# Kernel tuning notes

Hardware: AMD Instinct MI355X
Metric: run time of the kernel (lower is better)

## Reference

```python
import jax, jax.numpy as jnp
import numpy as np

N = 50000          # nodes
E = 1_600_000      # edges (avg degree 32)
IN = 128           # in_channels
H1, C1 = 4, 8      # conv1: heads=4, out=8 -> concat 32
OUT = 64           # out_channels (conv2, heads=1)
NEG_SLOPE = 0.2    # PyG GATConv default LeakyReLU slope


def _gat_layer(x, edge_index, W, att_src, att_dst, bias, heads, out_ch):
    """PyG-style GATConv (concat=True, add_self_loops=True).
    x: [N, F_in], edge_index: [2, E], W: [F_in, heads*out_ch],
    att_src/att_dst: [heads, out_ch], bias: [heads*out_ch].
    """
    n = x.shape[0]
    loops = jnp.arange(n)
    src = jnp.concatenate([edge_index[0], loops])  # message source j
    dst = jnp.concatenate([edge_index[1], loops])  # aggregation target i

    h = (x @ W).reshape(n, heads, out_ch)                 # [N, H, C]
    a_src = jnp.sum(h * att_src, axis=-1)                 # [N, H]
    a_dst = jnp.sum(h * att_dst, axis=-1)                 # [N, H]

    logits = jax.nn.leaky_relu(a_src[src] + a_dst[dst], NEG_SLOPE)  # [E', H]
    # segment softmax over incoming edges of each destination node
    m = jax.ops.segment_max(logits, dst, num_segments=n)            # [N, H]
    e = jnp.exp(logits - m[dst])
    s = jax.ops.segment_sum(e, dst, num_segments=n)                 # [N, H]
    alpha = e / (s[dst] + 1e-16)                                    # [E', H]

    msg = h[src] * alpha[..., None]                                 # [E', H, C]
    out = jax.ops.segment_sum(msg, dst, num_segments=n)             # [N, H, C]
    return out.reshape(n, heads * out_ch) + bias


def setup_inputs() -> dict:
    key = jax.random.key(0)
    ks = jax.random.split(key, 10)
    g = 0.1
    x = jax.random.normal(ks[0], (N, IN), jnp.float32)
    edge_index = jax.random.randint(ks[1], (2, E), 0, N, dtype=jnp.int64)
    W1 = jax.random.normal(ks[2], (IN, H1 * C1), jnp.float32) * g
    att_src1 = jax.random.normal(ks[3], (H1, C1), jnp.float32) * g
    att_dst1 = jax.random.normal(ks[4], (H1, C1), jnp.float32) * g
    b1 = jnp.zeros((H1 * C1,), jnp.float32)
    W2 = jax.random.normal(ks[5], (H1 * C1, OUT), jnp.float32) * g
    att_src2 = jax.random.normal(ks[6], (1, OUT), jnp.float32) * g
    att_dst2 = jax.random.normal(ks[7], (1, OUT), jnp.float32) * g
    b2 = jnp.zeros((OUT,), jnp.float32)
    return {"x": x, "edge_index": edge_index,
            "W1": W1, "att_src1": att_src1, "att_dst1": att_dst1, "b1": b1,
            "W2": W2, "att_src2": att_src2, "att_dst2": att_dst2, "b2": b2}


def reference(x, edge_index, W1, att_src1, att_dst1, b1, W2, att_src2, att_dst2, b2):
    h = _gat_layer(x, edge_index, W1, att_src1, att_dst1, b1, H1, C1)   # [N, 32]
    h = jax.nn.relu(h)
    out = _gat_layer(h, edge_index, W2, att_src2, att_dst2, b2, 1, OUT)  # [N, 64]
    return out
```

## Files before the change

### kernel.cpp

```cpp
#include <hip/hip_runtime.h>
#include <hip/hip_bf16.h>

#define IN_CH 128
#define H1C1  32
#define NH1   4
#define OUTC  64
#define NEG   0.2f
#define RPAD  16
#define BSH   6
#define BSZ   64
#define NBMAX 1024
#define CHUNK 4096
#define CAP   3072
#define PCAP  4096
#define NPB   32

typedef __hip_bfloat16 bf16;
typedef unsigned int u32;
typedef unsigned short u16;

__device__ __forceinline__ u16 f2bf_bits(float f) {
  bf16 v = __float2bfloat16(f);
  return *(u16*)&v;
}
__device__ __forceinline__ float bflo(u32 g) { return __uint_as_float(g << 16); }
__device__ __forceinline__ float bfhi(u32 g) { return __uint_as_float(g & 0xFFFF0000u); }

__global__ __launch_bounds__(256) void k_bin_tr(
    const int* __restrict__ ei, int* __restrict__ bucket_fill,
    u32* __restrict__ data, int E, int n, int nb, int nA,
    const float* __restrict__ x, const float* __restrict__ W1,
    const float* __restrict__ as1, const float* __restrict__ ad1,
    u16* __restrict__ h1b, float* __restrict__ a_src, float* __restrict__ a_dst) {
  __shared__ __align__(16) char smem[28672];
  int t = threadIdx.x;
  if ((int)blockIdx.x < nA) {
    int* cnt   = (int*)smem;
    int* lbase = cnt + NBMAX;
    int* gbase = lbase + NBMAX;
    u32* staged = (u32*)(gbase + NBMAX);
    int lane = t & 63, wid = t >> 6;
    for (int b = t; b < nb; b += 256) cnt[b] = 0;
    __syncthreads();
    long base = (long)blockIdx.x * CHUNK;
    long totE = (long)E + n;
    u32 pk[CHUNK / 256];
    int bk[CHUNK / 256];
#pragma unroll
    for (int i = 0; i < CHUNK / 256; i++) {
      long e = base + i * 256 + t;
      if (e < totE) {
        int j, d;
        if (e < E) {
          j = ei[e]; d = ei[E + e];
          j = j < 0 ? 0 : (j >= n ? n - 1 : j);
          d = d < 0 ? 0 : (d >= n ? n - 1 : d);
        } else { j = d = (int)(e - E); }
        bk[i] = d >> BSH;
        pk[i] = ((u32)d << 16) | (u32)j;
        atomicAdd(&cnt[bk[i]], 1);
      } else bk[i] = -1;
    }
    __syncthreads();
    if (wid == 0) {
      int carry = 0;
      for (int b0 = 0; b0 < nb; b0 += 64) {
        int i = b0 + lane;
        int v = (i < nb) ? cnt[i] : 0;
        int orig = v;
        for (int off = 1; off < 64; off <<= 1) {
          int u = __shfl_up(v, off, 64);
          if (lane >= off) v += u;
        }
        if (i < nb) lbase[i] = carry + v - orig;
        carry += __shfl(v, 63, 64);
      }
    }
    __syncthreads();
    for (int b = t; b < nb; b += 256) {
      int c = cnt[b];
      gbase[b] = c ? atomicAdd(&bucket_fill[b], c) : 0;
      cnt[b] = 0;
    }
    __syncthreads();
#pragma unroll
    for (int i = 0; i < CHUNK / 256; i++) {
      if (bk[i] >= 0) {
        int loc = atomicAdd(&cnt[bk[i]], 1);
        staged[lbase[bk[i]] + loc] = pk[i];
      }
    }
    __syncthreads();
    long remL = totE - base;
    int rem = remL > CHUNK ? CHUNK : (int)remL;
    for (int idx = t; idx < rem; idx += 256) {
      u32 p = staged[idx];
      int b = (int)(p >> 16) >> BSH;
      int off2 = gbase[b] + (idx - lbase[b]);
      if (off2 < CAP) data[(size_t)b * CAP + off2] = p;
    }
  } else {
    float* xs = (float*)smem;
    int base = ((int)blockIdx.x - nA) * NPB;
    for (int i4 = t; i4 < NPB * 32; i4 += 256) {
      int nd = base + (i4 >> 5);
      float4 v = make_float4(0.f, 0.f, 0.f, 0.f);
      if (nd < n) v = ((const float4*)x)[(size_t)base * 32 + i4];
      ((float4*)xs)[i4] = v;
    }
    int mg = t & 7, ks = (t >> 3) & 7, ns = t >> 6;
    int m0 = mg * 4;
    float4 w[4][4];
#pragma unroll
    for (int kk = 0; kk < 4; kk++) {
      int q = (kk + ks) & 3;
      int k0 = ks * 16 + q * 4;
      float4 t0 = *(const float4*)(W1 + (k0 + 0) * H1C1 + m0);
      float4 t1 = *(const float4*)(W1 + (k0 + 1) * H1C1 + m0);
      float4 t2 = *(const float4*)(W1 + (k0 + 2) * H1C1 + m0);
      float4 t3 = *(const float4*)(W1 + (k0 + 3) * H1C1 + m0);
      w[kk][0] = make_float4(t0.x, t1.x, t2.x, t3.x);
      w[kk][1] = make_float4(t0.y, t1.y, t2.y, t3.y);
      w[kk][2] = make_float4(t0.z, t1.z, t2.z, t3.z);
      w[kk][3] = make_float4(t0.w, t1.w, t2.w, t3.w);
    }
    float4 asq = *(const float4*)(as1 + m0);
    float4 adq = *(const float4*)(ad1 + m0);
    __syncthreads();
#pragma unroll 2
    for (int r = 0; r < 8; r++) {
      int nl = r * 4 + ns;
      const float4* xrow = (const float4*)(xs + nl * IN_CH + ks * 16);
      float a0 = 0.f, a1 = 0.f, a2 = 0.f, a3 = 0.f;
#pragma unroll
      for (int kk = 0; kk < 4; kk++) {
        int q = (kk + ks) & 3;
        float4 xv = xrow[q];
        a0 += xv.x * w[kk][0].x + xv.y * w[kk][0].y + xv.z * w[kk][0].z + xv.w * w[kk][0].w;
        a1 += xv.x * w[kk][1].x + xv.y * w[kk][1].y + xv.z * w[kk][1].z + xv.w * w[kk][1].w;
        a2 += xv.x * w[kk][2].x + xv.y * w[kk][2].y + xv.z * w[kk][2].z + xv.w * w[kk][2].w;
        a3 += xv.x * w[kk][3].x + xv.y * w[kk][3].y + xv.z * w[kk][3].z + xv.w * w[kk][3].w;
      }
#pragma unroll
      for (int off = 8; off < 64; off <<= 1) {
        a0 += __shfl_xor(a0, off, 64);
        a1 += __shfl_xor(a1, off, 64);
        a2 += __shfl_xor(a2, off, 64);
        a3 += __shfl_xor(a3, off, 64);
      }
      int node = base + nl;
      if (ks == 0 && node < n) {
        float vs = a0 * asq.x + a1 * asq.y + a2 * asq.z + a3 * asq.w;
        float vd = a0 * adq.x + a1 * adq.y + a2 * adq.z + a3 * adq.w;
        vs += __shfl_xor(vs, 1, 64);
        vd += __shfl_xor(vd, 1, 64);
        u32 lo = (u32)f2bf_bits(a0) | ((u32)f2bf_bits(a1) << 16);
        u32 hi = (u32)f2bf_bits(a2) | ((u32)f2bf_bits(a3) << 16);
        *(uint2*)(h1b + (size_t)node * H1C1 + m0) = make_uint2(lo, hi);
        if ((mg & 1) == 0) {
          a_src[node * NH1 + (mg >> 1)] = vs;
          a_dst[node * NH1 + (mg >> 1)] = vd;
        }
      }
    }
    if ((int)blockIdx.x == nA) {
      if (t < H1C1) h1b[n * H1C1 + t] = 0;
      if (t < NH1)  a_src[n * NH1 + t] = -1e30f;
    }
  }
}

__global__ __launch_bounds__(256) void k_bucket_scatter(
    const u32* __restrict__ data, const int* __restrict__ bucket_fill,
    int2* __restrict__ rowse, int* __restrict__ col, int n) {
  __shared__ int cur[BSZ];
  __shared__ int rp[BSZ];
  __shared__ int pd[BSZ];
  int t = threadIdx.x;
  int b = blockIdx.x;
  if (t < BSZ) cur[t] = 0;
  __syncthreads();
  int s = b * CAP;
  int cnt = bucket_fill[b];
  if (cnt > CAP) cnt = CAP;
  for (int i = t; i < cnt; i += 256)
    atomicAdd(&cur[(data[s + i] >> 16) & (BSZ - 1)], 1);
  __syncthreads();
  if (t < 64) {
    int raw = cur[t];
    int v = (raw + RPAD - 1) & ~(RPAD - 1);
    int orig = v;
    for (int off = 1; off < 64; off <<= 1) {
      int u = __shfl_up(v, off, 64);
      if (t >= off) v += u;
    }
    int r = b * PCAP + v - orig;
    rp[t] = r;
    pd[t] = orig;
    cur[t] = r;
    int node = (b << BSH) + t;
    if (node < n) rowse[node] = make_int2(r, r + orig);
  }
  __syncthreads();
  for (int i = t; i < cnt; i += 256) {
    u32 p = data[s + i];
    int dl = (int)(p >> 16) & (BSZ - 1);
    int pos = atomicAdd(&cur[dl], 1);
    col[pos] = (int)(p & 0xFFFFu);
  }
  __syncthreads();
  if (t < 64) {
    int c = cur[t];
    int end = rp[t] + pd[t];
    for (int k = c; k < end; k++) col[k] = n;
  }
}

__global__ __launch_bounds__(256) void k_l1_agg(
    const int2* __restrict__ rowse, const int* __restrict__ col,
    const u16* __restrict__ h1b, const float* __restrict__ a_src,
    const float* __restrict__ a_dst, const float* __restrict__ b1,
    const float* __restrict__ W2, const float* __restrict__ as2,
    const float* __restrict__ ad2,
    u16* __restrict__ h2, float* __restrict__ a_src2, float* __restrict__ a_dst2,
    int n) {
  __shared__ float W2s[8 * 256];
  __shared__ float hsh[16][H1C1];
  __shared__ int   js[4][4][64];
  __shared__ float wsh[4][4][NH1][68];
  int t = threadIdx.x;
  int wid = t >> 6, lane = t & 63;
  {
    int c = t & 63;
#pragma unroll
    for (int g = 0; g < 2; g++) {
      int kg = (t >> 6) + 4 * g;
      float4 v;
      v.x = W2[(kg * 4 + 0) * OUTC + c];
      v.y = W2[(kg * 4 + 1) * OUTC + c];
      v.z = W2[(kg * 4 + 2) * OUTC + c];
      v.w = W2[(kg * 4 + 3) * OUTC + c];
      *(float4*)(W2s + kg * 256 + c * 4) = v;
    }
  }
  int o = lane >> 3, u = lane & 7;
  int hd = u >> 1;
  const char* h1p = (const char*)h1b + 8 * u;
  int node0 = blockIdx.x * 16 + wid * 4;
  int rs[4], re[4], jv[4];
  float4 adv[4];
#pragma unroll
  for (int s = 0; s < 4; s++) {
    int nd = node0 + s;
    int2 se = make_int2(0, 0);
    if (nd < n) se = rowse[nd];
    rs[s] = se.x; re[s] = se.y;
  }
#pragma unroll
  for (int s = 0; s < 4; s++) {
    int k1 = re[s] - rs[s]; if (k1 > 64) k1 = 64;
    jv[s] = (lane < k1) ? col[rs[s] + lane] : n;
  }
#pragma unroll
  for (int s = 0; s < 4; s++) {
    int nd = node0 + s; int ndc = nd < n ? nd : 0;
    adv[s] = *(const float4*)(a_dst + ndc * NH1);
  }
  float4 asv[4];
#pragma unroll
  for (int s = 0; s < 4; s++) asv[s] = *(const float4*)(a_src + jv[s] * NH1);
#pragma unroll
  for (int s = 0; s < 4; s++) {
    float l0 = asv[s].x + adv[s].x; l0 = l0 > 0.f ? l0 : NEG * l0;
    float l1 = asv[s].y + adv[s].y; l1 = l1 > 0.f ? l1 : NEG * l1;
    float l2 = asv[s].z + adv[s].z; l2 = l2 > 0.f ? l2 : NEG * l2;
    float l3 = asv[s].w + adv[s].w; l3 = l3 > 0.f ? l3 : NEG * l3;
    js[wid][s][lane] = jv[s] << 6;
    wsh[wid][s][0][lane] = __expf(l0);
    wsh[wid][s][1][lane] = __expf(l1);
    wsh[wid][s][2][lane] = __expf(l2);
    wsh[wid][s][3][lane] = __expf(l3);
  }
#pragma unroll
  for (int s = 0; s < 4; s++) {
    float a0 = 0.f, a1 = 0.f, a2 = 0.f, a3 = 0.f, sw = 0.f;
    int k1 = re[s] - rs[s]; if (k1 > 64) k1 = 64;
    int nbod = k1 >> 4;
    uint2 G0[4], G1[4];
    float W0[4], W1v[4];
#pragma unroll
    for (int b = 0; b < 4; b++) {
      if (b < nbod) {
        int k = b * 16;
        int j0 = js[wid][s][k + o];
        int j1 = js[wid][s][k + 8 + o];
        W0[b]  = wsh[wid][s][hd][k + o];
        W1v[b] = wsh[wid][s][hd][k + 8 + o];
        G0[b] = *(const uint2*)(h1p + j0);
        G1[b] = *(const uint2*)(h1p + j1);
      }
    }
#pragma unroll
    for (int b = 0; b < 4; b++) {
      if (b < nbod) {
        float w0 = W0[b], w1 = W1v[b];
        uint2 g0 = G0[b], g1 = G1[b];
        a0 += w0 * bflo(g0.x) + w1 * bflo(g1.x);
        a1 += w0 * bfhi(g0.x) + w1 * bfhi(g1.x);
        a2 += w0 * bflo(g0.y) + w1 * bflo(g1.y);
        a3 += w0 * bfhi(g0.y) + w1 * bfhi(g1.y);
        sw += w0 + w1;
      }
    }
    for (int tb = rs[s] + 64; tb < re[s]; tb += 64) {
      int kmax = re[s] - tb; if (kmax > 64) kmax = 64;
      int jx = (lane < kmax) ? col[tb + lane] : n;
      float4 as = *(const float4*)(a_src + jx * NH1);
      float l0 = as.x + adv[s].x; l0 = l0 > 0.f ? l0 : NEG * l0;
      float l1 = as.y + adv[s].y; l1 = l1 > 0.f ? l1 : NEG * l1;
      float l2 = as.z + adv[s].z; l2 = l2 > 0.f ? l2 : NEG * l2;
      float l3 = as.w + adv[s].w; l3 = l3 > 0.f ? l3 : NEG * l3;
      js[wid][s][lane] = jx << 6;
      wsh[wid][s][0][lane] = __expf(l0);
      wsh[wid][s][1][lane] = __expf(l1);
      wsh[wid][s][2][lane] = __expf(l2);
      wsh[wid][s][3][lane] = __expf(l3);
      int nb2 = kmax >> 4;
#pragma unroll
      for (int b = 0; b < 4; b++) {
        if (b < nb2) {
          int k = b * 16;
          int j0 = js[wid][s][k + o];
          int j1 = js[wid][s][k + 8 + o];
          float w0 = wsh[wid][s][hd][k + o];
          float w1 = wsh[wid][s][hd][k + 8 + o];
          uint2 g0 = *(const uint2*)(h1p + j0);
          uint2 g1 = *(const uint2*)(h1p + j1);
          a0 += w0 * bflo(g0.x) + w1 * bflo(g1.x);
          a1 += w0 * bfhi(g0.x) + w1 * bfhi(g1.x);
          a2 += w0 * bflo(g0.y) + w1 * bflo(g1.y);
          a3 += w0 * bfhi(g0.y) + w1 * bfhi(g1.y);
          sw += w0 + w1;
        }
      }
    }
    for (int off = 8; off < 64; off <<= 1) {
      a0 += __shfl_xor(a0, off, 64);
      a1 += __shfl_xor(a1, off, 64);
      a2 += __shfl_xor(a2, off, 64);
      a3 += __shfl_xor(a3, off, 64);
      sw += __shfl_xor(sw, off, 64);
    }
    if (o == 0) {
      float inv = 1.f / (sw + 1e-16f);
      int c = 4 * u;
      hsh[wid * 4 + s][c]     = fmaxf(a0 * inv + b1[c], 0.f);
      hsh[wid * 4 + s][c + 1] = fmaxf(a1 * inv + b1[c + 1], 0.f);
      hsh[wid * 4 + s][c + 2] = fmaxf(a2 * inv + b1[c + 2], 0.f);
      hsh[wid * 4 + s][c + 3] = fmaxf(a3 * inv + b1[c + 3], 0.f);
    }
  }
  __syncthreads();
  float as2l = as2[lane], ad2l = ad2[lane];
  for (int r = 0; r < 4; r++) {
    int nl = wid * 4 + r;
    int node = blockIdx.x * 16 + nl;
    float acc = 0.f;
#pragma unroll
    for (int kg = 0; kg < 8; kg++) {
      float4 hv = *(const float4*)(&hsh[nl][kg * 4]);
      float4 wv = *(const float4*)(W2s + kg * 256 + lane * 4);
      acc += hv.x * wv.x + hv.y * wv.y + hv.z * wv.z + hv.w * wv.w;
    }
    float vs = acc * as2l;
    float vd = acc * ad2l;
    for (int off = 1; off < 64; off <<= 1) {
      vs += __shfl_xor(vs, off, 64);
      vd += __shfl_xor(vd, off, 64);
    }
    if (node < n) {
      h2[node * OUTC + lane] = f2bf_bits(acc);
      if (lane == 0) { a_src2[node] = vs; a_dst2[node] = vd; }
    }
  }
  if (blockIdx.x == 0) {
    if (t < OUTC) h2[n * OUTC + t] = 0;
    if (t == 0)   a_src2[n] = -1e30f;
  }
}

__global__ __launch_bounds__(256) void k_l2_agg(
    const int2* __restrict__ rowse, const int* __restrict__ col,
    const u16* __restrict__ h2, const float* __restrict__ a_src2,
    const float* __restrict__ a_dst2, const float* __restrict__ b2v,
    float* __restrict__ out, int n) {
  __shared__ int   js[4][4][64];
  __shared__ float wsh[4][4][64];
  int t = threadIdx.x;
  int wid = t >> 6, lane = t & 63;
  int o = lane >> 4, u = lane & 15;
  const char* h2p = (const char*)h2 + 8 * u;
  int node0 = blockIdx.x * 16 + wid * 4;
  int rs[4], re[4], jv[4];
  float adv[4];
#pragma unroll
  for (int s = 0; s < 4; s++) {
    int nd = node0 + s;
    int2 se = make_int2(0, 0);
    if (nd < n) se = rowse[nd];
    rs[s] = se.x; re[s] = se.y;
  }
#pragma unroll
  for (int s = 0; s < 4; s++) {
    int k1 = re[s] - rs[s]; if (k1 > 64) k1 = 64;
    jv[s] = (lane < k1) ? col[rs[s] + lane] : n;
  }
#pragma unroll
  for (int s = 0; s < 4; s++) {
    int nd = node0 + s; int ndc = nd < n ? nd : 0;
    adv[s] = a_dst2[ndc];
  }
  float asv[4];
#pragma unroll
  for (int s = 0; s < 4; s++) asv[s] = a_src2[jv[s]];
#pragma unroll
  for (int s = 0; s < 4; s++) {
    float lg = asv[s] + adv[s];
    lg = lg > 0.f ? lg : NEG * lg;
    js[wid][s][lane] = jv[s] << 7;
    wsh[wid][s][lane] = __expf(lg);
  }
#pragma unroll
  for (int s = 0; s < 4; s++) {
    int node = node0 + s;
    float a0 = 0.f, a1 = 0.f, a2 = 0.f, a3 = 0.f, sw = 0.f;
    int k1 = re[s] - rs[s]; if (k1 > 64) k1 = 64;
    int nbod = k1 >> 4;
    uint2 G[4][4];
    float W[4][4];
#pragma unroll
    for (int b = 0; b < 4; b++) {
      if (b < nbod) {
#pragma unroll
        for (int q = 0; q < 4; q++) {
          int e = b * 16 + 4 * q + o;
          W[b][q] = wsh[wid][s][e];
          G[b][q] = *(const uint2*)(h2p + js[wid][s][e]);
        }
      }
    }
#pragma unroll
    for (int b = 0; b < 4; b++) {
      if (b < nbod) {
        a0 += W[b][0] * bflo(G[b][0].x) + W[b][1] * bflo(G[b][1].x);
        a0 += W[b][2] * bflo(G[b][2].x) + W[b][3] * bflo(G[b][3].x);
        a1 += W[b][0] * bfhi(G[b][0].x) + W[b][1] * bfhi(G[b][1].x);
        a1 += W[b][2] * bfhi(G[b][2].x) + W[b][3] * bfhi(G[b][3].x);
        a2 += W[b][0] * bflo(G[b][0].y) + W[b][1] * bflo(G[b][1].y);
        a2 += W[b][2] * bflo(G[b][2].y) + W[b][3] * bflo(G[b][3].y);
        a3 += W[b][0] * bfhi(G[b][0].y) + W[b][1] * bfhi(G[b][1].y);
        a3 += W[b][2] * bfhi(G[b][2].y) + W[b][3] * bfhi(G[b][3].y);
        sw += (W[b][0] + W[b][1]) + (W[b][2] + W[b][3]);
      }
    }
    for (int tb = rs[s] + 64; tb < re[s]; tb += 64) {
      int kmax = re[s] - tb; if (kmax > 64) kmax = 64;
      int jx = (lane < kmax) ? col[tb + lane] : n;
      float lg = a_src2[jx] + adv[s];
      lg = lg > 0.f ? lg : NEG * lg;
      js[wid][s][lane] = jx << 7;
      wsh[wid][s][lane] = __expf(lg);
      int nb2 = kmax >> 4;
#pragma unroll
      for (int b = 0; b < 4; b++) {
        if (b < nb2) {
          float w0, w1, w2, w3;
          uint2 g0, g1, g2, g3;
          int k = b * 16;
          w0 = wsh[wid][s][k + o];      g0 = *(const uint2*)(h2p + js[wid][s][k + o]);
          w1 = wsh[wid][s][k + 4 + o];  g1 = *(const uint2*)(h2p + js[wid][s][k + 4 + o]);
          w2 = wsh[wid][s][k + 8 + o];  g2 = *(const uint2*)(h2p + js[wid][s][k + 8 + o]);
          w3 = wsh[wid][s][k + 12 + o]; g3 = *(const uint2*)(h2p + js[wid][s][k + 12 + o]);
          a0 += w0 * bflo(g0.x) + w1 * bflo(g1.x) + w2 * bflo(g2.x) + w3 * bflo(g3.x);
          a1 += w0 * bfhi(g0.x) + w1 * bfhi(g1.x) + w2 * bfhi(g2.x) + w3 * bfhi(g3.x);
          a2 += w0 * bflo(g0.y) + w1 * bflo(g1.y) + w2 * bflo(g2.y) + w3 * bflo(g3.y);
          a3 += w0 * bfhi(g0.y) + w1 * bfhi(g1.y) + w2 * bfhi(g2.y) + w3 * bfhi(g3.y);
          sw += (w0 + w1) + (w2 + w3);
        }
      }
    }
    for (int off = 16; off < 64; off <<= 1) {
      a0 += __shfl_xor(a0, off, 64);
      a1 += __shfl_xor(a1, off, 64);
      a2 += __shfl_xor(a2, off, 64);
      a3 += __shfl_xor(a3, off, 64);
      sw += __shfl_xor(sw, off, 64);
    }
    if (o == 0 && node < n) {
      float inv = 1.f / (sw + 1e-16f);
      int c = 4 * u;
      float4 ov;
      ov.x = a0 * inv + b2v[c];
      ov.y = a1 * inv + b2v[c + 1];
      ov.z = a2 * inv + b2v[c + 2];
      ov.w = a3 * inv + b2v[c + 3];
      *(float4*)(out + node * OUTC + c) = ov;
    }
  }
}


extern "C" void kernel_launch(void* const* d_in, const int* in_sizes, int n_in,
                              void* d_out, int out_size, void* d_ws, size_t ws_size,
                              hipStream_t stream) {
  const float* x   = (const float*)d_in[0];
  const int*   ei  = (const int*)d_in[1];
  const float* W1  = (const float*)d_in[2];
  const float* as1 = (const float*)d_in[3];
  const float* ad1 = (const float*)d_in[4];
  const float* b1  = (const float*)d_in[5];
  const float* W2  = (const float*)d_in[6];
  const float* as2 = (const float*)d_in[7];
  const float* ad2 = (const float*)d_in[8];
  const float* b2  = (const float*)d_in[9];
  float* out = (float*)d_out;

  int n = in_sizes[0] / IN_CH;
  int E = in_sizes[1] / 2;
  int nb = (n + BSZ - 1) >> BSH;
  long tot = (long)E + n;
  int nA = (int)((tot + CHUNK - 1) / CHUNK);
  int nTr = (n + NPB - 1) / NPB;

  char* w = (char*)d_ws;
  auto al = [](size_t v) { return (v + 255) & ~(size_t)255; };
  size_t off = 0;
  int*  bucket_fill = (int*)(w + off);  off += al((size_t)nb * 4);
  int2* rowse       = (int2*)(w + off); off += al((size_t)(n + 1) * 8);
  u32*  data        = (u32*)(w + off);  off += al((size_t)nb * CAP * 4);
  int*  col         = (int*)(w + off);  off += al((size_t)nb * PCAP * 4);
  u16*  h1b         = (u16*)(w + off);  off += al((size_t)(n + 1) * H1C1 * 2);
  float* a_src1     = (float*)(w + off); off += al((size_t)(n + 1) * NH1 * 4);
  float* a_dst1     = (float*)(w + off); off += al((size_t)(n + 1) * NH1 * 4);
  u16*  h2          = (u16*)(w + off);  off += al((size_t)(n + 1) * OUTC * 2);
  float* a_src2     = (float*)(w + off); off += al((size_t)(n + 1) * 4);
  float* a_dst2     = (float*)(w + off); off += al((size_t)(n + 1) * 4);

  hipMemsetAsync(bucket_fill, 0, (size_t)nb * 4, stream);
  hipLaunchKernelGGL(k_bin_tr, dim3(nA + nTr), dim3(256), 0, stream,
                     ei, bucket_fill, data, E, n, nb, nA,
                     x, W1, as1, ad1, h1b, a_src1, a_dst1);
  hipLaunchKernelGGL(k_bucket_scatter, dim3(nb), dim3(256), 0, stream,
                     data, bucket_fill, rowse, col, n);

  hipLaunchKernelGGL(k_l1_agg, dim3((n + 15) / 16), dim3(256), 0, stream,
                     rowse, col, h1b, a_src1, a_dst1, b1,
                     W2, as2, ad2, h2, a_src2, a_dst2, n);

  hipLaunchKernelGGL(k_l2_agg, dim3((n + 15) / 16), dim3(256), 0, stream,
                     rowse, col, h2, a_src2, a_dst2, b2, out, n);
}
```

Baseline: 212.4 us.

## Build fixed-capacity per-node adjacency with global atomics instead of bucket-sort CSR

Replaces the two-stage bucket sort (local histogram, prefix scan, staged scatter, plus a separate per-bucket scatter kernel) with a direct per-destination atomic slot claim into a padded adjacency array of 128 entries per node. This removes one kernel launch and the intermediate bucket buffer pass. The aggregation kernels now read the per-node degree and index the row directly, rounding the batch count up instead of relying on padded sentinel columns. In exchange it issues many contended global atomics with return values, writes scattered 4-byte column entries into a larger array, and silently drops any in-edges beyond 128 per node.

```diff
diff --git a/kernel.cpp b/kernel.cpp
--- a/kernel.cpp
+++ b/kernel.cpp
@@ -6,13 +6,8 @@
 #define NH1   4
 #define OUTC  64
 #define NEG   0.2f
-#define RPAD  16
-#define BSH   6
-#define BSZ   64
-#define NBMAX 1024
+#define DMAX  128
 #define CHUNK 4096
-#define CAP   3072
-#define PCAP  4096
 #define NPB   32
 
 typedef __hip_bfloat16 bf16;
@@ -27,25 +22,16 @@
 __device__ __forceinline__ float bfhi(u32 g) { return __uint_as_float(g & 0xFFFF0000u); }
 
 __global__ __launch_bounds__(256) void k_bin_tr(
-    const int* __restrict__ ei, int* __restrict__ bucket_fill,
-    u32* __restrict__ data, int E, int n, int nb, int nA,
+    const int* __restrict__ ei, int* __restrict__ deg, int* __restrict__ col,
+    int E, int n, int nA,
     const float* __restrict__ x, const float* __restrict__ W1,
     const float* __restrict__ as1, const float* __restrict__ ad1,
     u16* __restrict__ h1b, float* __restrict__ a_src, float* __restrict__ a_dst) {
-  __shared__ __align__(16) char smem[28672];
+  __shared__ __align__(16) float xs[NPB * IN_CH];
   int t = threadIdx.x;
   if ((int)blockIdx.x < nA) {
-    int* cnt   = (int*)smem;
-    int* lbase = cnt + NBMAX;
-    int* gbase = lbase + NBMAX;
-    u32* staged = (u32*)(gbase + NBMAX);
-    int lane = t & 63, wid = t >> 6;
-    for (int b = t; b < nb; b += 256) cnt[b] = 0;
-    __syncthreads();
     long base = (long)blockIdx.x * CHUNK;
     long totE = (long)E + n;
-    u32 pk[CHUNK / 256];
-    int bk[CHUNK / 256];
 #pragma unroll
     for (int i = 0; i < CHUNK / 256; i++) {
       long e = base + i * 256 + t;
@@ -56,51 +42,11 @@
           j = j < 0 ? 0 : (j >= n ? n - 1 : j);
           d = d < 0 ? 0 : (d >= n ? n - 1 : d);
         } else { j = d = (int)(e - E); }
-        bk[i] = d >> BSH;
-        pk[i] = ((u32)d << 16) | (u32)j;
-        atomicAdd(&cnt[bk[i]], 1);
-      } else bk[i] = -1;
-    }
-    __syncthreads();
-    if (wid == 0) {
-      int carry = 0;
-      for (int b0 = 0; b0 < nb; b0 += 64) {
-        int i = b0 + lane;
-        int v = (i < nb) ? cnt[i] : 0;
-        int orig = v;
-        for (int off = 1; off < 64; off <<= 1) {
-          int u = __shfl_up(v, off, 64);
-          if (lane >= off) v += u;
-        }
-        if (i < nb) lbase[i] = carry + v - orig;
-        carry += __shfl(v, 63, 64);
-      }
-    }
-    __syncthreads();
-    for (int b = t; b < nb; b += 256) {
-      int c = cnt[b];
-      gbase[b] = c ? atomicAdd(&bucket_fill[b], c) : 0;
-      cnt[b] = 0;
-    }
-    __syncthreads();
-#pragma unroll
-    for (int i = 0; i < CHUNK / 256; i++) {
-      if (bk[i] >= 0) {
-        int loc = atomicAdd(&cnt[bk[i]], 1);
-        staged[lbase[bk[i]] + loc] = pk[i];
-      }
-    }
-    __syncthreads();
-    long remL = totE - base;
-    int rem = remL > CHUNK ? CHUNK : (int)remL;
-    for (int idx = t; idx < rem; idx += 256) {
-      u32 p = staged[idx];
-      int b = (int)(p >> 16) >> BSH;
-      int off2 = gbase[b] + (idx - lbase[b]);
-      if (off2 < CAP) data[(size_t)b * CAP + off2] = p;
+        int pos = atomicAdd(&deg[d], 1);
+        if (pos < DMAX) col[(d << 7) + pos] = j;
+      }
     }
   } else {
-    float* xs = (float*)smem;
     int base = ((int)blockIdx.x - nA) * NPB;
     for (int i4 = t; i4 < NPB * 32; i4 += 256) {
       int nd = base + (i4 >> 5);
@@ -170,54 +116,8 @@
   }
 }
 
-__global__ __launch_bounds__(256) void k_bucket_scatter(
-    const u32* __restrict__ data, const int* __restrict__ bucket_fill,
-    int2* __restrict__ rowse, int* __restrict__ col, int n) {
-  __shared__ int cur[BSZ];
-  __shared__ int rp[BSZ];
-  __shared__ int pd[BSZ];
-  int t = threadIdx.x;
-  int b = blockIdx.x;
-  if (t < BSZ) cur[t] = 0;
-  __syncthreads();
-  int s = b * CAP;
-  int cnt = bucket_fill[b];
-  if (cnt > CAP) cnt = CAP;
-  for (int i = t; i < cnt; i += 256)
-    atomicAdd(&cur[(data[s + i] >> 16) & (BSZ - 1)], 1);
-  __syncthreads();
-  if (t < 64) {
-    int raw = cur[t];
-    int v = (raw + RPAD - 1) & ~(RPAD - 1);
-    int orig = v;
-    for (int off = 1; off < 64; off <<= 1) {
-      int u = __shfl_up(v, off, 64);
-      if (t >= off) v += u;
-    }
-    int r = b * PCAP + v - orig;
-    rp[t] = r;
-    pd[t] = orig;
-    cur[t] = r;
-    int node = (b << BSH) + t;
-    if (node < n) rowse[node] = make_int2(r, r + orig);
-  }
-  __syncthreads();
-  for (int i = t; i < cnt; i += 256) {
-    u32 p = data[s + i];
-    int dl = (int)(p >> 16) & (BSZ - 1);
-    int pos = atomicAdd(&cur[dl], 1);
-    col[pos] = (int)(p & 0xFFFFu);
-  }
-  __syncthreads();
-  if (t < 64) {
-    int c = cur[t];
-    int end = rp[t] + pd[t];
-    for (int k = c; k < end; k++) col[k] = n;
-  }
-}
-
 __global__ __launch_bounds__(256) void k_l1_agg(
-    const int2* __restrict__ rowse, const int* __restrict__ col,
+    const int* __restrict__ deg, const int* __restrict__ col,
     const u16* __restrict__ h1b, const float* __restrict__ a_src,
     const float* __restrict__ a_dst, const float* __restrict__ b1,
     const float* __restrict__ W2, const float* __restrict__ as2,
@@ -247,24 +147,28 @@
   int hd = u >> 1;
   const char* h1p = (const char*)h1b + 8 * u;
   int node0 = blockIdx.x * 16 + wid * 4;
-  int rs[4], re[4], jv[4];
+  int dg[4], cv[4], jv[4];
   float4 adv[4];
 #pragma unroll
   for (int s = 0; s < 4; s++) {
     int nd = node0 + s;
-    int2 se = make_int2(0, 0);
-    if (nd < n) se = rowse[nd];
-    rs[s] = se.x; re[s] = se.y;
-  }
-#pragma unroll
-  for (int s = 0; s < 4; s++) {
-    int k1 = re[s] - rs[s]; if (k1 > 64) k1 = 64;
-    jv[s] = (lane < k1) ? col[rs[s] + lane] : n;
+    int d = (nd < n) ? deg[nd] : 0;
+    dg[s] = d > DMAX ? DMAX : d;
+  }
+#pragma unroll
+  for (int s = 0; s < 4; s++) {
+    int ndc = (node0 + s) < n ? (node0 + s) : 0;
+    cv[s] = col[(ndc << 7) + lane];
   }
 #pragma unroll
   for (int s = 0; s < 4; s++) {
     int nd = node0 + s; int ndc = nd < n ? nd : 0;
     adv[s] = *(const float4*)(a_dst + ndc * NH1);
+  }
+#pragma unroll
+  for (int s = 0; s < 4; s++) {
+    int k1 = dg[s] > 64 ? 64 : dg[s];
+    jv[s] = (lane < k1) ? cv[s] : n;
   }
   float4 asv[4];
 #pragma unroll
@@ -284,8 +188,8 @@
 #pragma unroll
   for (int s = 0; s < 4; s++) {
     float a0 = 0.f, a1 = 0.f, a2 = 0.f, a3 = 0.f, sw = 0.f;
-    int k1 = re[s] - rs[s]; if (k1 > 64) k1 = 64;
-    int nbod = k1 >> 4;
+    int k1 = dg[s] > 64 ? 64 : dg[s];
+    int nbod = (k1 + 15) >> 4;
     uint2 G0[4], G1[4];
     float W0[4], W1v[4];
 #pragma unroll
@@ -312,9 +216,10 @@
         sw += w0 + w1;
       }
     }
-    for (int tb = rs[s] + 64; tb < re[s]; tb += 64) {
-      int kmax = re[s] - tb; if (kmax > 64) kmax = 64;
-      int jx = (lane < kmax) ? col[tb + lane] : n;
+    for (int tb = 64; tb < dg[s]; tb += 64) {
+      int kmax = dg[s] - tb; if (kmax > 64) kmax = 64;
+      int node = node0 + s;
+      int jx = (lane < kmax) ? col[(node << 7) + tb + lane] : n;
       float4 as = *(const float4*)(a_src + jx * NH1);
       float l0 = as.x + adv[s].x; l0 = l0 > 0.f ? l0 : NEG * l0;
       float l1 = as.y + adv[s].y; l1 = l1 > 0.f ? l1 : NEG * l1;
@@ -325,7 +230,7 @@
       wsh[wid][s][1][lane] = __expf(l1);
       wsh[wid][s][2][lane] = __expf(l2);
       wsh[wid][s][3][lane] = __expf(l3);
-      int nb2 = kmax >> 4;
+      int nb2 = (kmax + 15) >> 4;
 #pragma unroll
       for (int b = 0; b < 4; b++) {
         if (b < nb2) {
@@ -390,7 +295,7 @@
 }
 
 __global__ __launch_bounds__(256) void k_l2_agg(
-    const int2* __restrict__ rowse, const int* __restrict__ col,
+    const int* __restrict__ deg, const int* __restrict__ col,
     const u16* __restrict__ h2, const float* __restrict__ a_src2,
     const float* __restrict__ a_dst2, const float* __restrict__ b2v,
     float* __restrict__ out, int n) {
@@ -401,24 +306,28 @@
   int o = lane >> 4, u = lane & 15;
   const char* h2p = (const char*)h2 + 8 * u;
   int node0 = blockIdx.x * 16 + wid * 4;
-  int rs[4], re[4], jv[4];
+  int dg[4], cv[4], jv[4];
   float adv[4];
 #pragma unroll
   for (int s = 0; s < 4; s++) {
     int nd = node0 + s;
-    int2 se = make_int2(0, 0);
-    if (nd < n) se = rowse[nd];
-    rs[s] = se.x; re[s] = se.y;
-  }
-#pragma unroll
-  for (int s = 0; s < 4; s++) {
-    int k1 = re[s] - rs[s]; if (k1 > 64) k1 = 64;
-    jv[s] = (lane < k1) ? col[rs[s] + lane] : n;
+    int d = (nd < n) ? deg[nd] : 0;
+    dg[s] = d > DMAX ? DMAX : d;
+  }
+#pragma unroll
+  for (int s = 0; s < 4; s++) {
+    int ndc = (node0 + s) < n ? (node0 + s) : 0;
+    cv[s] = col[(ndc << 7) + lane];
   }
 #pragma unroll
   for (int s = 0; s < 4; s++) {
     int nd = node0 + s; int ndc = nd < n ? nd : 0;
     adv[s] = a_dst2[ndc];
+  }
+#pragma unroll
+  for (int s = 0; s < 4; s++) {
+    int k1 = dg[s] > 64 ? 64 : dg[s];
+    jv[s] = (lane < k1) ? cv[s] : n;
   }
   float asv[4];
 #pragma unroll
@@ -434,8 +343,8 @@
   for (int s = 0; s < 4; s++) {
     int node = node0 + s;
     float a0 = 0.f, a1 = 0.f, a2 = 0.f, a3 = 0.f, sw = 0.f;
-    int k1 = re[s] - rs[s]; if (k1 > 64) k1 = 64;
-    int nbod = k1 >> 4;
+    int k1 = dg[s] > 64 ? 64 : dg[s];
+    int nbod = (k1 + 15) >> 4;
     uint2 G[4][4];
     float W[4][4];
 #pragma unroll
@@ -463,14 +372,14 @@
         sw += (W[b][0] + W[b][1]) + (W[b][2] + W[b][3]);
       }
     }
-    for (int tb = rs[s] + 64; tb < re[s]; tb += 64) {
-      int kmax = re[s] - tb; if (kmax > 64) kmax = 64;
-      int jx = (lane < kmax) ? col[tb + lane] : n;
+    for (int tb = 64; tb < dg[s]; tb += 64) {
+      int kmax = dg[s] - tb; if (kmax > 64) kmax = 64;
+      int jx = (lane < kmax) ? col[(node << 7) + tb + lane] : n;
       float lg = a_src2[jx] + adv[s];
       lg = lg > 0.f ? lg : NEG * lg;
       js[wid][s][lane] = jx << 7;
       wsh[wid][s][lane] = __expf(lg);
-      int nb2 = kmax >> 4;
+      int nb2 = (kmax + 15) >> 4;
 #pragma unroll
       for (int b = 0; b < 4; b++) {
         if (b < nb2) {
@@ -527,7 +436,6 @@
 
   int n = in_sizes[0] / IN_CH;
   int E = in_sizes[1] / 2;
-  int nb = (n + BSZ - 1) >> BSH;
   long tot = (long)E + n;
   int nA = (int)((tot + CHUNK - 1) / CHUNK);
   int nTr = (n + NPB - 1) / NPB;
@@ -535,10 +443,8 @@
   char* w = (char*)d_ws;
   auto al = [](size_t v) { return (v + 255) & ~(size_t)255; };
   size_t off = 0;
-  int*  bucket_fill = (int*)(w + off);  off += al((size_t)nb * 4);
-  int2* rowse       = (int2*)(w + off); off += al((size_t)(n + 1) * 8);
-  u32*  data        = (u32*)(w + off);  off += al((size_t)nb * CAP * 4);
-  int*  col         = (int*)(w + off);  off += al((size_t)nb * PCAP * 4);
+  int*  deg         = (int*)(w + off);  off += al((size_t)(n + 1) * 4);
+  int*  col         = (int*)(w + off);  off += al((size_t)n * DMAX * 4);
   u16*  h1b         = (u16*)(w + off);  off += al((size_t)(n + 1) * H1C1 * 2);
   float* a_src1     = (float*)(w + off); off += al((size_t)(n + 1) * NH1 * 4);
   float* a_dst1     = (float*)(w + off); off += al((size_t)(n + 1) * NH1 * 4);
@@ -546,17 +452,15 @@
   float* a_src2     = (float*)(w + off); off += al((size_t)(n + 1) * 4);
   float* a_dst2     = (float*)(w + off); off += al((size_t)(n + 1) * 4);
 
-  hipMemsetAsync(bucket_fill, 0, (size_t)nb * 4, stream);
+  hipMemsetAsync(deg, 0, (size_t)n * 4, stream);
   hipLaunchKernelGGL(k_bin_tr, dim3(nA + nTr), dim3(256), 0, stream,
-                     ei, bucket_fill, data, E, n, nb, nA,
+                     ei, deg, col, E, n, nA,
                      x, W1, as1, ad1, h1b, a_src1, a_dst1);
-  hipLaunchKernelGGL(k_bucket_scatter, dim3(nb), dim3(256), 0, stream,
-                     data, bucket_fill, rowse, col, n);
 
   hipLaunchKernelGGL(k_l1_agg, dim3((n + 15) / 16), dim3(256), 0, stream,
-                     rowse, col, h1b, a_src1, a_dst1, b1,
+                     deg, col, h1b, a_src1, a_dst1, b1,
                      W2, as2, ad2, h2, a_src2, a_dst2, n);
 
   hipLaunchKernelGGL(k_l2_agg, dim3((n + 15) / 16), dim3(256), 0, stream,
-                     rowse, col, h2, a_src2, a_dst2, b2, out, n);
+                     deg, col, h2, a_src2, a_dst2, b2, out, n);
 }
```

New measurement: 257.0 us. +21.0%, slower.

## Give each 16-lane group one node in the GAT aggregation kernels

Applied to the files above, without the earlier changes.

Both aggregation kernels now give each 16-lane group of a wave its own destination node. Each lane walks that node's edges eight at a time, reading neighbour indices straight from global memory with vector loads and attention weights from shared memory. This removes the shared index buffer, the per-node serial loop and the cross-lane shuffle reductions, and edges beyond the first 64 are handled by a per-lane scalar tail. Row padding drops from 16 to 8 and a capacity constant shrinks to match. In exchange, each lane runs a serial dependent chain over the degree, and warps diverge when node degrees differ.

```diff
diff --git a/kernel.cpp b/kernel.cpp
--- a/kernel.cpp
+++ b/kernel.cpp
@@ -6,13 +6,13 @@
 #define NH1   4
 #define OUTC  64
 #define NEG   0.2f
-#define RPAD  16
+#define RPAD  8
 #define BSH   6
 #define BSZ   64
 #define NBMAX 1024
 #define CHUNK 4096
 #define CAP   3072
-#define PCAP  4096
+#define PCAP  3584
 #define NPB   32
 
 typedef __hip_bfloat16 bf16;
@@ -226,7 +226,6 @@
     int n) {
   __shared__ float W2s[8 * 256];
   __shared__ float hsh[16][H1C1];
-  __shared__ int   js[4][4][64];
   __shared__ float wsh[4][4][NH1][68];
   int t = threadIdx.x;
   int wid = t >> 6, lane = t & 63;
@@ -243,9 +242,6 @@
       *(float4*)(W2s + kg * 256 + c * 4) = v;
     }
   }
-  int o = lane >> 3, u = lane & 7;
-  int hd = u >> 1;
-  const char* h1p = (const char*)h1b + 8 * u;
   int node0 = blockIdx.x * 16 + wid * 4;
   int rs[4], re[4], jv[4];
   float4 adv[4];
@@ -275,90 +271,56 @@
     float l1 = asv[s].y + adv[s].y; l1 = l1 > 0.f ? l1 : NEG * l1;
     float l2 = asv[s].z + adv[s].z; l2 = l2 > 0.f ? l2 : NEG * l2;
     float l3 = asv[s].w + adv[s].w; l3 = l3 > 0.f ? l3 : NEG * l3;
-    js[wid][s][lane] = jv[s] << 6;
     wsh[wid][s][0][lane] = __expf(l0);
     wsh[wid][s][1][lane] = __expf(l1);
     wsh[wid][s][2][lane] = __expf(l2);
     wsh[wid][s][3][lane] = __expf(l3);
   }
-#pragma unroll
-  for (int s = 0; s < 4; s++) {
-    float a0 = 0.f, a1 = 0.f, a2 = 0.f, a3 = 0.f, sw = 0.f;
-    int k1 = re[s] - rs[s]; if (k1 > 64) k1 = 64;
-    int nbod = k1 >> 4;
-    uint2 G0[4], G1[4];
-    float W0[4], W1v[4];
-#pragma unroll
-    for (int b = 0; b < 4; b++) {
-      if (b < nbod) {
-        int k = b * 16;
-        int j0 = js[wid][s][k + o];
-        int j1 = js[wid][s][k + 8 + o];
-        W0[b]  = wsh[wid][s][hd][k + o];
-        W1v[b] = wsh[wid][s][hd][k + 8 + o];
-        G0[b] = *(const uint2*)(h1p + j0);
-        G1[b] = *(const uint2*)(h1p + j1);
-      }
-    }
-#pragma unroll
-    for (int b = 0; b < 4; b++) {
-      if (b < nbod) {
-        float w0 = W0[b], w1 = W1v[b];
-        uint2 g0 = G0[b], g1 = G1[b];
-        a0 += w0 * bflo(g0.x) + w1 * bflo(g1.x);
-        a1 += w0 * bfhi(g0.x) + w1 * bfhi(g1.x);
-        a2 += w0 * bflo(g0.y) + w1 * bflo(g1.y);
-        a3 += w0 * bfhi(g0.y) + w1 * bfhi(g1.y);
-        sw += w0 + w1;
-      }
-    }
-    for (int tb = rs[s] + 64; tb < re[s]; tb += 64) {
-      int kmax = re[s] - tb; if (kmax > 64) kmax = 64;
-      int jx = (lane < kmax) ? col[tb + lane] : n;
-      float4 as = *(const float4*)(a_src + jx * NH1);
-      float l0 = as.x + adv[s].x; l0 = l0 > 0.f ? l0 : NEG * l0;
-      float l1 = as.y + adv[s].y; l1 = l1 > 0.f ? l1 : NEG * l1;
-      float l2 = as.z + adv[s].z; l2 = l2 > 0.f ? l2 : NEG * l2;
-      float l3 = as.w + adv[s].w; l3 = l3 > 0.f ? l3 : NEG * l3;
-      js[wid][s][lane] = jx << 6;
-      wsh[wid][s][0][lane] = __expf(l0);
-      wsh[wid][s][1][lane] = __expf(l1);
-      wsh[wid][s][2][lane] = __expf(l2);
-      wsh[wid][s][3][lane] = __expf(l3);
-      int nb2 = kmax >> 4;
-#pragma unroll
-      for (int b = 0; b < 4; b++) {
-        if (b < nb2) {
-          int k = b * 16;
-          int j0 = js[wid][s][k + o];
-          int j1 = js[wid][s][k + 8 + o];
-          float w0 = wsh[wid][s][hd][k + o];
-          float w1 = wsh[wid][s][hd][k + 8 + o];
-          uint2 g0 = *(const uint2*)(h1p + j0);
-          uint2 g1 = *(const uint2*)(h1p + j1);
-          a0 += w0 * bflo(g0.x) + w1 * bflo(g1.x);
-          a1 += w0 * bfhi(g0.x) + w1 * bfhi(g1.x);
-          a2 += w0 * bflo(g0.y) + w1 * bflo(g1.y);
-          a3 += w0 * bfhi(g0.y) + w1 * bfhi(g1.y);
-          sw += w0 + w1;
-        }
-      }
-    }
-    for (int off = 8; off < 64; off <<= 1) {
-      a0 += __shfl_xor(a0, off, 64);
-      a1 += __shfl_xor(a1, off, 64);
-      a2 += __shfl_xor(a2, off, 64);
-      a3 += __shfl_xor(a3, off, 64);
-      sw += __shfl_xor(sw, off, 64);
-    }
-    if (o == 0) {
-      float inv = 1.f / (sw + 1e-16f);
-      int c = 4 * u;
-      hsh[wid * 4 + s][c]     = fmaxf(a0 * inv + b1[c], 0.f);
-      hsh[wid * 4 + s][c + 1] = fmaxf(a1 * inv + b1[c + 1], 0.f);
-      hsh[wid * 4 + s][c + 2] = fmaxf(a2 * inv + b1[c + 2], 0.f);
-      hsh[wid * 4 + s][c + 3] = fmaxf(a3 * inv + b1[c + 3], 0.f);
-    }
+  int s_me = lane >> 4, u = lane & 15, hd = u >> 2;
+  int node_me = node0 + s_me;
+  int2 seme = (node_me < n) ? rowse[node_me] : make_int2(0, 0);
+  int rs_me = seme.x, klen = seme.y - seme.x;
+  int k1 = klen > 64 ? 64 : klen;
+  const int* colp = col + rs_me;
+  const char* h1p = (const char*)h1b + 4 * u;
+  const float* wrow = &wsh[wid][s_me][hd][0];
+  float a0 = 0.f, a1 = 0.f, sw = 0.f;
+  for (int kb = 0; kb < k1; kb += 8) {
+    int4 c0 = *(const int4*)(colp + kb);
+    int4 c1 = *(const int4*)(colp + kb + 4);
+    u32 g0 = *(const u32*)(h1p + (c0.x << 6));
+    u32 g1 = *(const u32*)(h1p + (c0.y << 6));
+    u32 g2 = *(const u32*)(h1p + (c0.z << 6));
+    u32 g3 = *(const u32*)(h1p + (c0.w << 6));
+    u32 g4 = *(const u32*)(h1p + (c1.x << 6));
+    u32 g5 = *(const u32*)(h1p + (c1.y << 6));
+    u32 g6 = *(const u32*)(h1p + (c1.z << 6));
+    u32 g7 = *(const u32*)(h1p + (c1.w << 6));
+    float4 wa = *(const float4*)(wrow + kb);
+    float4 wb = *(const float4*)(wrow + kb + 4);
+    a0 += wa.x * bflo(g0) + wa.y * bflo(g1) + wa.z * bflo(g2) + wa.w * bflo(g3);
+    a1 += wa.x * bfhi(g0) + wa.y * bfhi(g1) + wa.z * bfhi(g2) + wa.w * bfhi(g3);
+    a0 += wb.x * bflo(g4) + wb.y * bflo(g5) + wb.z * bflo(g6) + wb.w * bflo(g7);
+    a1 += wb.x * bfhi(g4) + wb.y * bfhi(g5) + wb.z * bfhi(g6) + wb.w * bfhi(g7);
+    sw += (wa.x + wa.y) + (wa.z + wa.w) + (wb.x + wb.y) + (wb.z + wb.w);
+  }
+  if (klen > 64) {
+    float ad_hd = a_dst[node_me * NH1 + hd];
+    for (int e = 64; e < klen; e++) {
+      int j = colp[e];
+      float as = a_src[j * NH1 + hd];
+      float lg = as + ad_hd; lg = lg > 0.f ? lg : NEG * lg;
+      float wv = __expf(lg);
+      u32 g = *(const u32*)(h1p + (j << 6));
+      a0 += wv * bflo(g); a1 += wv * bfhi(g); sw += wv;
+    }
+  }
+  {
+    float inv = 1.f / (sw + 1e-16f);
+    int c = 2 * u;
+    float r0 = fmaxf(a0 * inv + b1[c], 0.f);
+    float r1 = fmaxf(a1 * inv + b1[c + 1], 0.f);
+    *(float2*)(&hsh[wid * 4 + s_me][c]) = make_float2(r0, r1);
   }
   __syncthreads();
   float as2l = as2[lane], ad2l = ad2[lane];
@@ -394,12 +356,9 @@
     const u16* __restrict__ h2, const float* __restrict__ a_src2,
     const float* __restrict__ a_dst2, const float* __restrict__ b2v,
     float* __restrict__ out, int n) {
-  __shared__ int   js[4][4][64];
-  __shared__ float wsh[4][4][64];
+  __shared__ float wsh[4][4][68];
   int t = threadIdx.x;
   int wid = t >> 6, lane = t & 63;
-  int o = lane >> 4, u = lane & 15;
-  const char* h2p = (const char*)h2 + 8 * u;
   int node0 = blockIdx.x * 16 + wid * 4;
   int rs[4], re[4], jv[4];
   float adv[4];
@@ -427,85 +386,61 @@
   for (int s = 0; s < 4; s++) {
     float lg = asv[s] + adv[s];
     lg = lg > 0.f ? lg : NEG * lg;
-    js[wid][s][lane] = jv[s] << 7;
     wsh[wid][s][lane] = __expf(lg);
   }
-#pragma unroll
-  for (int s = 0; s < 4; s++) {
-    int node = node0 + s;
-    float a0 = 0.f, a1 = 0.f, a2 = 0.f, a3 = 0.f, sw = 0.f;
-    int k1 = re[s] - rs[s]; if (k1 > 64) k1 = 64;
-    int nbod = k1 >> 4;
-    uint2 G[4][4];
-    float W[4][4];
-#pragma unroll
-    for (int b = 0; b < 4; b++) {
-      if (b < nbod) {
-#pragma unroll
-        for (int q = 0; q < 4; q++) {
-          int e = b * 16 + 4 * q + o;
-          W[b][q] = wsh[wid][s][e];
-          G[b][q] = *(const uint2*)(h2p + js[wid][s][e]);
-        }
-      }
-    }
-#pragma unroll
-    for (int b = 0; b < 4; b++) {
-      if (b < nbod) {
-        a0 += W[b][0] * bflo(G[b][0].x) + W[b][1] * bflo(G[b][1].x);
-        a0 += W[b][2] * bflo(G[b][2].x) + W[b][3] * bflo(G[b][3].x);
-        a1 += W[b][0] * bfhi(G[b][0].x) + W[b][1] * bfhi(G[b][1].x);
-        a1 += W[b][2] * bfhi(G[b][2].x) + W[b][3] * bfhi(G[b][3].x);
-        a2 += W[b][0] * bflo(G[b][0].y) + W[b][1] * bflo(G[b][1].y);
-        a2 += W[b][2] * bflo(G[b][2].y) + W[b][3] * bflo(G[b][3].y);
-        a3 += W[b][0] * bfhi(G[b][0].y) + W[b][1] * bfhi(G[b][1].y);
-        a3 += W[b][2] * bfhi(G[b][2].y) + W[b][3] * bfhi(G[b][3].y);
-        sw += (W[b][0] + W[b][1]) + (W[b][2] + W[b][3]);
-      }
-    }
-    for (int tb = rs[s] + 64; tb < re[s]; tb += 64) {
-      int kmax = re[s] - tb; if (kmax > 64) kmax = 64;
-      int jx = (lane < kmax) ? col[tb + lane] : n;
-      float lg = a_src2[jx] + adv[s];
-      lg = lg > 0.f ? lg : NEG * lg;
-      js[wid][s][lane] = jx << 7;
-      wsh[wid][s][lane] = __expf(lg);
-      int nb2 = kmax >> 4;
-#pragma unroll
-      for (int b = 0; b < 4; b++) {
-        if (b < nb2) {
-          float w0, w1, w2, w3;
-          uint2 g0, g1, g2, g3;
-          int k = b * 16;
-          w0 = wsh[wid][s][k + o];      g0 = *(const uint2*)(h2p + js[wid][s][k + o]);
-          w1 = wsh[wid][s][k + 4 + o];  g1 = *(const uint2*)(h2p + js[wid][s][k + 4 + o]);
-          w2 = wsh[wid][s][k + 8 + o];  g2 = *(const uint2*)(h2p + js[wid][s][k + 8 + o]);
-          w3 = wsh[wid][s][k + 12 + o]; g3 = *(const uint2*)(h2p + js[wid][s][k + 12 + o]);
-          a0 += w0 * bflo(g0.x) + w1 * bflo(g1.x) + w2 * bflo(g2.x) + w3 * bflo(g3.x);
-          a1 += w0 * bfhi(g0.x) + w1 * bfhi(g1.x) + w2 * bfhi(g2.x) + w3 * bfhi(g3.x);
-          a2 += w0 * bflo(g0.y) + w1 * bflo(g1.y) + w2 * bflo(g2.y) + w3 * bflo(g3.y);
-          a3 += w0 * bfhi(g0.y) + w1 * bfhi(g1.y) + w2 * bfhi(g2.y) + w3 * bfhi(g3.y);
-          sw += (w0 + w1) + (w2 + w3);
-        }
-      }
-    }
-    for (int off = 16; off < 64; off <<= 1) {
-      a0 += __shfl_xor(a0, off, 64);
-      a1 += __shfl_xor(a1, off, 64);
-      a2 += __shfl_xor(a2, off, 64);
-      a3 += __shfl_xor(a3, off, 64);
-      sw += __shfl_xor(sw, off, 64);
-    }
-    if (o == 0 && node < n) {
-      float inv = 1.f / (sw + 1e-16f);
-      int c = 4 * u;
-      float4 ov;
-      ov.x = a0 * inv + b2v[c];
-      ov.y = a1 * inv + b2v[c + 1];
-      ov.z = a2 * inv + b2v[c + 2];
-      ov.w = a3 * inv + b2v[c + 3];
-      *(float4*)(out + node * OUTC + c) = ov;
-    }
+  int s_me = lane >> 4, u = lane & 15;
+  int node_me = node0 + s_me;
+  int2 seme = (node_me < n) ? rowse[node_me] : make_int2(0, 0);
+  int rs_me = seme.x, klen = seme.y - seme.x;
+  int k1 = klen > 64 ? 64 : klen;
+  const int* colp = col + rs_me;
+  const char* h2p = (const char*)h2 + 8 * u;
+  const float* wrow = &wsh[wid][s_me][0];
+  float a0 = 0.f, a1 = 0.f, a2 = 0.f, a3 = 0.f, sw = 0.f;
+  for (int kb = 0; kb < k1; kb += 8) {
+    int4 c0 = *(const int4*)(colp + kb);
+    int4 c1 = *(const int4*)(colp + kb + 4);
+    uint2 g0 = *(const uint2*)(h2p + (c0.x << 7));
+    uint2 g1 = *(const uint2*)(h2p + (c0.y << 7));
+    uint2 g2 = *(const uint2*)(h2p + (c0.z << 7));
+    uint2 g3 = *(const uint2*)(h2p + (c0.w << 7));
+    uint2 g4 = *(const uint2*)(h2p + (c1.x << 7));
+    uint2 g5 = *(const uint2*)(h2p + (c1.y << 7));
+    uint2 g6 = *(const uint2*)(h2p + (c1.z << 7));
+    uint2 g7 = *(const uint2*)(h2p + (c1.w << 7));
+    float4 wa = *(const float4*)(wrow + kb);
+    float4 wb = *(const float4*)(wrow + kb + 4);
+    a0 += wa.x * bflo(g0.x) + wa.y * bflo(g1.x) + wa.z * bflo(g2.x) + wa.w * bflo(g3.x);
+    a1 += wa.x * bfhi(g0.x) + wa.y * bfhi(g1.x) + wa.z * bfhi(g2.x) + wa.w * bfhi(g3.x);
+    a2 += wa.x * bflo(g0.y) + wa.y * bflo(g1.y) + wa.z * bflo(g2.y) + wa.w * bflo(g3.y);
+    a3 += wa.x * bfhi(g0.y) + wa.y * bfhi(g1.y) + wa.z * bfhi(g2.y) + wa.w * bfhi(g3.y);
+    a0 += wb.x * bflo(g4.x) + wb.y * bflo(g5.x) + wb.z * bflo(g6.x) + wb.w * bflo(g7.x);
+    a1 += wb.x * bfhi(g4.x) + wb.y * bfhi(g5.x) + wb.z * bfhi(g6.x) + wb.w * bfhi(g7.x);
+    a2 += wb.x * bflo(g4.y) + wb.y * bflo(g5.y) + wb.z * bflo(g6.y) + wb.w * bflo(g7.y);
+    a3 += wb.x * bfhi(g4.y) + wb.y * bfhi(g5.y) + wb.z * bfhi(g6.y) + wb.w * bfhi(g7.y);
+    sw += (wa.x + wa.y) + (wa.z + wa.w) + (wb.x + wb.y) + (wb.z + wb.w);
+  }
+  if (klen > 64) {
+    float ad = a_dst2[node_me];
+    for (int e = 64; e < klen; e++) {
+      int j = colp[e];
+      float lg = a_src2[j] + ad; lg = lg > 0.f ? lg : NEG * lg;
+      float wv = __expf(lg);
+      uint2 g = *(const uint2*)(h2p + (j << 7));
+      a0 += wv * bflo(g.x); a1 += wv * bfhi(g.x);
+      a2 += wv * bflo(g.y); a3 += wv * bfhi(g.y);
+      sw += wv;
+    }
+  }
+  if (node_me < n) {
+    float inv = 1.f / (sw + 1e-16f);
+    int c = 4 * u;
+    float4 ov;
+    ov.x = a0 * inv + b2v[c];
+    ov.y = a1 * inv + b2v[c + 1];
+    ov.z = a2 * inv + b2v[c + 2];
+    ov.w = a3 * inv + b2v[c + 3];
+    *(float4*)(out + node_me * OUTC + c) = ov;
   }
 }
 
```

Result: faster. 203.7 us (-4.1%).
